# Performance work log

Measured on AMD Instinct MI355X. Metric: run time of the kernel, lower is better.

The kernel has to match this reference:

```python
import jax, jax.numpy as jnp
import numpy as np

B, C_IN, C_OUT, PODS = 32, 128, 128, 2
H_IN, W_IN = 56, 56
H_PAD, W_PAD = 64, 64  # next powers of 2


def hadamard_matrix(n):
    # Sylvester construction; n is a power of 2 (fixed small loop over log2 n)
    H = jnp.array([[1.0]], dtype=jnp.float32)
    base = jnp.array([[1.0, 1.0], [1.0, -1.0]], dtype=jnp.float32)
    for _ in range(int(np.log2(n))):
        H = jnp.kron(H, base)
    return H


def setup_inputs() -> dict:
    key = jax.random.key(0)
    k1, k2, k3, k4 = jax.random.split(key, 4)
    x = jax.random.normal(k1, (B, C_IN, H_IN, W_IN), dtype=jnp.float32)
    # grouped 1x1 conv weight, one (out,in) matrix per pod
    conv_w = jax.random.normal(k2, (PODS, C_OUT, C_IN), dtype=jnp.float32) / np.sqrt(C_IN)
    log_v = jnp.zeros((PODS, H_PAD, W_PAD), dtype=jnp.float32)
    T = jax.random.uniform(k3, (C_OUT, 1, 1), dtype=jnp.float32) / 10.0
    return {"x": x, "conv_w": conv_w, "log_v": log_v, "T": T}


def reference(x, conv_w, log_v, T):
    Hh = hadamard_matrix(H_PAD)  # symmetric
    Hw = hadamard_matrix(W_PAD)
    # pad spatial dims up to powers of 2
    f0 = jnp.pad(x, ((0, 0), (0, 0), (0, H_PAD - H_IN), (0, W_PAD - W_IN)))
    # WHT along W then H (H is symmetric so u @ H == H @ u along that axis)
    f1 = jnp.einsum('bchw,wk->bchk', f0, Hw)
    f2 = jnp.einsum('bchw,hk->bckw', f1, Hh)
    # per-pod frequency-domain scaling: (B,pods,C,H,W)
    v = jnp.exp(log_v)  # (pods,H,W)
    f2e = f2[:, None] * v[None, :, None]
    # grouped 1x1 conv (one GEMM per pod) + sum over pods
    f5 = jnp.einsum('bpihw,poi->bohw', f2e, conv_w)
    # per-channel soft thresholding
    thr = jax.nn.relu(T)  # (C_out,1,1)
    f6 = jnp.copysign(jax.nn.relu(jnp.abs(f5) - thr), f5)
    # inverse WHT (divide by n per axis)
    f7 = jnp.einsum('bchw,wk->bchk', f6, Hw) / W_PAD
    f8 = jnp.einsum('bchw,hk->bckw', f7, Hh) / H_PAD
    y = f8[..., :H_IN, :W_IN]
    # residual (C_in == C_out)
    return y + x
```

## Files before the change

kernel.cpp:

```cpp
#include <hip/hip_runtime.h>
#include <hip/hip_bf16.h>

using bf16x8  = __attribute__((ext_vector_type(8))) short;
using f32x4   = __attribute__((ext_vector_type(4))) float;
using ushort8 = __attribute__((ext_vector_type(8))) unsigned short;
using uint2v  = __attribute__((ext_vector_type(2))) unsigned int;

#define BB   32
#define CIN  128
#define COUT 128
#define PODS 2
#define HIN  56
#define WIN  56
#define HW   4096

__device__ __forceinline__ unsigned short bf16bits(float v) {
  __hip_bfloat16 h = __float2bfloat16(v);
  return reinterpret_cast<unsigned short&>(h);
}
__device__ __forceinline__ float bits2f(unsigned short u) {
  return __uint_as_float(((unsigned)u) << 16);
}

template<int LEN>
__device__ __forceinline__ void fwht_stage(float (&a)[64]) {
  #pragma unroll
  for (int i = 0; i < 64; i += 2*LEN) {
    #pragma unroll
    for (int j = 0; j < LEN; ++j) {
      float u = a[i+j], v = a[i+j+LEN];
      a[i+j]     = u + v;
      a[i+j+LEN] = u - v;
    }
  }
}
__device__ __forceinline__ void fwht64(float (&a)[64]) {
  fwht_stage<1>(a); fwht_stage<2>(a); fwht_stage<4>(a);
  fwht_stage<8>(a); fwht_stage<16>(a); fwht_stage<32>(a);
}

__global__ void k_wconv(const float* __restrict__ w, unsigned short* __restrict__ Wb) {
  int i = blockIdx.x * 256 + threadIdx.x;
  if (i < PODS*COUT*CIN) Wb[i] = bf16bits(w[i]);
}

__global__ __launch_bounds__(64) void k_fwht_fwd(const float* __restrict__ x,
                                                 unsigned short* __restrict__ F) {
  const int bc   = blockIdx.x;
  const int lane = threadIdx.x;
  const float* xp = x + (size_t)bc * (HIN*WIN);

  float a[64];
  #pragma unroll
  for (int h = 0; h < 64; ++h) a[h] = 0.f;
  if (lane < WIN) {
    #pragma unroll
    for (int h = 0; h < HIN; ++h) a[h] = xp[h*WIN + lane];
  }
  fwht64(a);

  __shared__ float t[64][65];
  #pragma unroll
  for (int k = 0; k < 64; ++k) t[k][lane] = a[k];
  __syncthreads();
  #pragma unroll
  for (int w = 0; w < 64; ++w) a[w] = t[lane][w];
  fwht64(a);

  unsigned short* Fp = F + (size_t)bc * HW + lane*64;
  #pragma unroll
  for (int j = 0; j < 8; ++j) {
    ushort8 v;
    #pragma unroll
    for (int e = 0; e < 8; ++e) v[e] = bf16bits(a[j*8 + e]);
    *reinterpret_cast<ushort8*>(Fp + j*8) = v;
  }
}

__global__ __launch_bounds__(256, 2) void k_mix(const unsigned short* F,
                                                const unsigned short* __restrict__ Wb,
                                                const float* __restrict__ lv,
                                                const float* __restrict__ T,
                                                unsigned short* G) {
  const int b    = blockIdx.x >> 5;
  const int hwb  = blockIdx.x & 31;
  const int tid  = threadIdx.x;
  const int wave = tid >> 6;
  const int l    = tid & 63;

  __shared__ __align__(16) char Blds[PODS][32768];

  const int arow = l & 15;
  const int acol = (l >> 4) * 8;
  bf16x8 afr[PODS][2][4];
  #pragma unroll
  for (int p = 0; p < PODS; ++p)
    #pragma unroll
    for (int tm = 0; tm < 2; ++tm)
      #pragma unroll
      for (int kk = 0; kk < 4; ++kk) {
        int o = wave*32 + tm*16 + arow;
        size_t off = ((size_t)(p*COUT + o))*CIN + kk*32 + acol;
        afr[p][tm][kk] = *reinterpret_cast<const bf16x8*>(Wb + off);
      }

  const int hwl  = (wave & 1)*64 + l;
  const int ib   = (wave >> 1)*64;
  const int hwg  = hwb*128 + hwl;
  const float v0 = expf(lv[hwg]);
  const float v1 = expf(lv[HW + hwg]);
  const unsigned short* Fb = F + (size_t)b * CIN * HW;
  const int rowbase = hwl * 256;
  const int sw      = (hwl & 7) << 4;
  #pragma unroll
  for (int it = 0; it < 16; ++it) {
    int i0 = ib + it*4;
    float f0 = bits2f(Fb[(size_t)(i0+0)*HW + hwg]);
    float f1 = bits2f(Fb[(size_t)(i0+1)*HW + hwg]);
    float f2 = bits2f(Fb[(size_t)(i0+2)*HW + hwg]);
    float f3 = bits2f(Fb[(size_t)(i0+3)*HW + hwg]);
    int boff = rowbase + ((i0*2) ^ sw);
    {
      unsigned r0 = (unsigned)bf16bits(f0*v0) | ((unsigned)bf16bits(f1*v0) << 16);
      unsigned r1 = (unsigned)bf16bits(f2*v0) | ((unsigned)bf16bits(f3*v0) << 16);
      uint2v val = {r0, r1};
      *reinterpret_cast<uint2v*>(&Blds[0][boff]) = val;
    }
    {
      unsigned r0 = (unsigned)bf16bits(f0*v1) | ((unsigned)bf16bits(f1*v1) << 16);
      unsigned r1 = (unsigned)bf16bits(f2*v1) | ((unsigned)bf16bits(f3*v1) << 16);
      uint2v val = {r0, r1};
      *reinterpret_cast<uint2v*>(&Blds[1][boff]) = val;
    }
  }
  __syncthreads();

  f32x4 acc[2][8];
  #pragma unroll
  for (int tm = 0; tm < 2; ++tm)
    #pragma unroll
    for (int t = 0; t < 8; ++t)
      acc[tm][t] = (f32x4){0.f, 0.f, 0.f, 0.f};

  #pragma unroll
  for (int t = 0; t < 8; ++t) {
    int row = t*16 + (l & 15);
    int rb  = row * 256;
    int s2  = (row & 7) << 4;
    #pragma unroll
    for (int kk = 0; kk < 4; ++kk) {
      int cb = (kk*64 + (l >> 4)*16) ^ s2;
      bf16x8 b0 = *reinterpret_cast<const bf16x8*>(&Blds[0][rb + cb]);
      bf16x8 b1 = *reinterpret_cast<const bf16x8*>(&Blds[1][rb + cb]);
      #pragma unroll
      for (int tm = 0; tm < 2; ++tm) {
        acc[tm][t] = __builtin_amdgcn_mfma_f32_16x16x32_bf16(afr[0][tm][kk], b0, acc[tm][t], 0, 0, 0);
        acc[tm][t] = __builtin_amdgcn_mfma_f32_16x16x32_bf16(afr[1][tm][kk], b1, acc[tm][t], 0, 0, 0);
      }
    }
  }

  unsigned short* Gb = G + (size_t)b * COUT * HW + hwb*128;
  #pragma unroll
  for (int tm = 0; tm < 2; ++tm) {
    #pragma unroll
    for (int r = 0; r < 4; ++r) {
      int o = wave*32 + tm*16 + (l >> 4)*4 + r;
      float th = fmaxf(T[o], 0.f);
      #pragma unroll
      for (int t = 0; t < 8; ++t) {
        float f = acc[tm][t][r];
        float m = fabsf(f) - th;
        m = m > 0.f ? m : 0.f;
        Gb[(size_t)o*HW + t*16 + (l & 15)] = bf16bits(copysignf(m, f));
      }
    }
  }
}

__global__ __launch_bounds__(64) void k_ifwht(const unsigned short* __restrict__ G,
                                              const float* __restrict__ x,
                                              float* __restrict__ y) {
  const int bo   = blockIdx.x;
  const int lane = threadIdx.x;
  const unsigned short* Gp = G + (size_t)bo * HW;

  float a[64];
  #pragma unroll
  for (int h = 0; h < 64; ++h) a[h] = bits2f(Gp[h*64 + lane]);
  fwht64(a);

  __shared__ float t[64][65];
  #pragma unroll
  for (int k = 0; k < 64; ++k) t[k][lane] = a[k];
  __syncthreads();
  #pragma unroll
  for (int w = 0; w < 64; ++w) a[w] = t[lane][w];
  fwht64(a);

  if (lane < HIN) {
    const float* xp = x + (size_t)bo*(HIN*WIN) + lane*WIN;
    float*       yp = y + (size_t)bo*(HIN*WIN) + lane*WIN;
    #pragma unroll
    for (int w4 = 0; w4 < 14; ++w4) {
      float4 xv = reinterpret_cast<const float4*>(xp)[w4];
      float4 r;
      r.x = a[w4*4+0]*(1.f/4096.f) + xv.x;
      r.y = a[w4*4+1]*(1.f/4096.f) + xv.y;
      r.z = a[w4*4+2]*(1.f/4096.f) + xv.z;
      r.w = a[w4*4+3]*(1.f/4096.f) + xv.w;
      reinterpret_cast<float4*>(yp)[w4] = r;
    }
  }
}

extern "C" void kernel_launch(void* const* d_in, const int* in_sizes, int n_in,
                              void* d_out, int out_size, void* d_ws, size_t ws_size,
                              hipStream_t stream) {
  const float* x  = (const float*)d_in[0];
  const float* cw = (const float*)d_in[1];
  const float* lv = (const float*)d_in[2];
  const float* T  = (const float*)d_in[3];
  float* y = (float*)d_out;

  char* ws = (char*)d_ws;
  const size_t szW = 65536;
  const size_t szF = (size_t)BB * CIN * HW * 2;
  const size_t szG = (size_t)BB * COUT * HW * 2;

  unsigned short* Wb = (unsigned short*)ws;
  unsigned short* F  = (unsigned short*)(ws + szW);
  unsigned short* G  = (ws_size >= szW + szF + szG)
                     ? (unsigned short*)(ws + szW + szF) : F;

  k_wconv   <<<dim3((PODS*COUT*CIN + 255)/256), dim3(256), 0, stream>>>(cw, Wb);
  k_fwht_fwd<<<dim3(BB*CIN),  dim3(64),  0, stream>>>(x, F);
  k_mix     <<<dim3(BB*32),   dim3(256), 0, stream>>>(F, Wb, lv, T, G);
  k_ifwht   <<<dim3(BB*COUT), dim3(64),  0, stream>>>(G, x, y);
}
```

Before: 83.95 us.

## Store spectrum transposed, vectorize row loads, fold weight conversion into mix

The forward WHT now loads each image row with contiguous float4 reads and runs the W transform first, so the intermediate spectrum is stored in transposed (w,h) order. The mix kernel remaps its log_v index to match, and the inverse kernel reads each lane's 64 values with contiguous 16-byte loads instead of strided scalar loads. The separate weight-to-bf16 kernel is removed and the mix kernel converts fp32 weights itself, saving one launch at the cost of redundant conversion work per block. The block barrier in the transpose is replaced by a bare lgkmcnt wait, which is only valid because each block is a single wave.

New measurement: 86.10 us. 2.6% more time.

```diff
diff --git a/kernel.cpp b/kernel.cpp
--- a/kernel.cpp
+++ b/kernel.cpp
@@ -39,32 +39,37 @@
   fwht_stage<8>(a); fwht_stage<16>(a); fwht_stage<32>(a);
 }
 
-__global__ void k_wconv(const float* __restrict__ w, unsigned short* __restrict__ Wb) {
-  int i = blockIdx.x * 256 + threadIdx.x;
-  if (i < PODS*COUT*CIN) Wb[i] = bf16bits(w[i]);
+__device__ __forceinline__ void transpose64(float (&a)[64], float (*t)[66], int lane) {
+  #pragma unroll
+  for (int w = 0; w < 64; ++w) t[lane][w] = a[w];
+  asm volatile("s_waitcnt lgkmcnt(0)" ::: "memory");
+  #pragma unroll
+  for (int k = 0; k < 64; ++k) a[k] = t[k][lane];
 }
 
 __global__ __launch_bounds__(64) void k_fwht_fwd(const float* __restrict__ x,
                                                  unsigned short* __restrict__ F) {
   const int bc   = blockIdx.x;
   const int lane = threadIdx.x;
-  const float* xp = x + (size_t)bc * (HIN*WIN);
 
   float a[64];
-  #pragma unroll
-  for (int h = 0; h < 64; ++h) a[h] = 0.f;
-  if (lane < WIN) {
-    #pragma unroll
-    for (int h = 0; h < HIN; ++h) a[h] = xp[h*WIN + lane];
-  }
-  fwht64(a);
-
-  __shared__ float t[64][65];
-  #pragma unroll
-  for (int k = 0; k < 64; ++k) t[k][lane] = a[k];
-  __syncthreads();
-  #pragma unroll
-  for (int w = 0; w < 64; ++w) a[w] = t[lane][w];
+  if (lane < HIN) {
+    const float4* xr = reinterpret_cast<const float4*>(x + (size_t)bc*(HIN*WIN) + lane*WIN);
+    #pragma unroll
+    for (int j = 0; j < 14; ++j) {
+      float4 v = xr[j];
+      a[j*4+0] = v.x; a[j*4+1] = v.y; a[j*4+2] = v.z; a[j*4+3] = v.w;
+    }
+    #pragma unroll
+    for (int w = WIN; w < 64; ++w) a[w] = 0.f;
+  } else {
+    #pragma unroll
+    for (int w = 0; w < 64; ++w) a[w] = 0.f;
+  }
+
+  fwht64(a);
+  __shared__ float t[64][66];
+  transpose64(a, t, lane);
   fwht64(a);
 
   unsigned short* Fp = F + (size_t)bc * HW + lane*64;
@@ -78,7 +83,7 @@
 }
 
 __global__ __launch_bounds__(256, 2) void k_mix(const unsigned short* F,
-                                                const unsigned short* __restrict__ Wb,
+                                                const float* __restrict__ cw,
                                                 const float* __restrict__ lv,
                                                 const float* __restrict__ T,
                                                 unsigned short* G) {
@@ -101,14 +106,22 @@
       for (int kk = 0; kk < 4; ++kk) {
         int o = wave*32 + tm*16 + arow;
         size_t off = ((size_t)(p*COUT + o))*CIN + kk*32 + acol;
-        afr[p][tm][kk] = *reinterpret_cast<const bf16x8*>(Wb + off);
+        float4 w0 = *reinterpret_cast<const float4*>(cw + off);
+        float4 w1 = *reinterpret_cast<const float4*>(cw + off + 4);
+        bf16x8 fr;
+        fr[0] = (short)bf16bits(w0.x); fr[1] = (short)bf16bits(w0.y);
+        fr[2] = (short)bf16bits(w0.z); fr[3] = (short)bf16bits(w0.w);
+        fr[4] = (short)bf16bits(w1.x); fr[5] = (short)bf16bits(w1.y);
+        fr[6] = (short)bf16bits(w1.z); fr[7] = (short)bf16bits(w1.w);
+        afr[p][tm][kk] = fr;
       }
 
   const int hwl  = (wave & 1)*64 + l;
   const int ib   = (wave >> 1)*64;
   const int hwg  = hwb*128 + hwl;
-  const float v0 = expf(lv[hwg]);
-  const float v1 = expf(lv[HW + hwg]);
+  const int ivs  = (hwg & 63)*64 + (hwg >> 6);
+  const float v0 = expf(lv[ivs]);
+  const float v1 = expf(lv[HW + ivs]);
   const unsigned short* Fb = F + (size_t)b * CIN * HW;
   const int rowbase = hwl * 256;
   const int sw      = (hwl & 7) << 4;
@@ -183,33 +196,33 @@
                                               float* __restrict__ y) {
   const int bo   = blockIdx.x;
   const int lane = threadIdx.x;
-  const unsigned short* Gp = G + (size_t)bo * HW;
+  const unsigned short* Gp = G + (size_t)bo * HW + lane*64;
 
   float a[64];
   #pragma unroll
-  for (int h = 0; h < 64; ++h) a[h] = bits2f(Gp[h*64 + lane]);
-  fwht64(a);
-
-  __shared__ float t[64][65];
-  #pragma unroll
-  for (int k = 0; k < 64; ++k) t[k][lane] = a[k];
-  __syncthreads();
-  #pragma unroll
-  for (int w = 0; w < 64; ++w) a[w] = t[lane][w];
+  for (int j = 0; j < 8; ++j) {
+    ushort8 g = *reinterpret_cast<const ushort8*>(Gp + j*8);
+    #pragma unroll
+    for (int e = 0; e < 8; ++e) a[j*8+e] = bits2f(g[e]);
+  }
+
+  fwht64(a);
+  __shared__ float t[64][66];
+  transpose64(a, t, lane);
   fwht64(a);
 
   if (lane < HIN) {
-    const float* xp = x + (size_t)bo*(HIN*WIN) + lane*WIN;
-    float*       yp = y + (size_t)bo*(HIN*WIN) + lane*WIN;
+    const float4* xr = reinterpret_cast<const float4*>(x + (size_t)bo*(HIN*WIN) + lane*WIN);
+    float4*       yr = reinterpret_cast<float4*>      (y + (size_t)bo*(HIN*WIN) + lane*WIN);
     #pragma unroll
     for (int w4 = 0; w4 < 14; ++w4) {
-      float4 xv = reinterpret_cast<const float4*>(xp)[w4];
+      float4 xv = xr[w4];
       float4 r;
       r.x = a[w4*4+0]*(1.f/4096.f) + xv.x;
       r.y = a[w4*4+1]*(1.f/4096.f) + xv.y;
       r.z = a[w4*4+2]*(1.f/4096.f) + xv.z;
       r.w = a[w4*4+3]*(1.f/4096.f) + xv.w;
-      reinterpret_cast<float4*>(yp)[w4] = r;
+      yr[w4] = r;
     }
   }
 }
@@ -224,17 +237,14 @@
   float* y = (float*)d_out;
 
   char* ws = (char*)d_ws;
-  const size_t szW = 65536;
   const size_t szF = (size_t)BB * CIN * HW * 2;
   const size_t szG = (size_t)BB * COUT * HW * 2;
 
-  unsigned short* Wb = (unsigned short*)ws;
-  unsigned short* F  = (unsigned short*)(ws + szW);
-  unsigned short* G  = (ws_size >= szW + szF + szG)
-                     ? (unsigned short*)(ws + szW + szF) : F;
-
-  k_wconv   <<<dim3((PODS*COUT*CIN + 255)/256), dim3(256), 0, stream>>>(cw, Wb);
+  unsigned short* F  = (unsigned short*)ws;
+  unsigned short* G  = (ws_size >= szF + szG)
+                     ? (unsigned short*)(ws + szF) : F;
+
   k_fwht_fwd<<<dim3(BB*CIN),  dim3(64),  0, stream>>>(x, F);
-  k_mix     <<<dim3(BB*32),   dim3(256), 0, stream>>>(F, Wb, lv, T, G);
+  k_mix     <<<dim3(BB*32),   dim3(256), 0, stream>>>(F, cw, lv, T, G);
   k_ifwht   <<<dim3(BB*COUT), dim3(64),  0, stream>>>(G, x, y);
 }
```
